# Optimization experiments

Hardware: AMD Instinct MI355X
Metric: run time of the kernel (lower is better)

Reference implementation:

```python
import jax, jax.numpy as jnp
import numpy as np

B, N, FIN, FOUT = 8, 2048, 128, 64
ALPHA = 0.2      # LeakyReLU negative slope
NEG_INF = -9e15  # matches torch constant -9000000000000000.0
LN_EPS = 1e-5


def setup_inputs() -> dict:
    key = jax.random.key(0)
    k1, k2, k3, k4 = jax.random.split(key, 4)
    x = jax.random.normal(k1, (B, N, FIN), dtype=jnp.float32)
    adj = jax.random.randint(k2, (B, N, N), 0, 2, dtype=jnp.int32)
    # params: W is nn.Linear(in,out,bias=False) -> stored here as [FIN,FOUT];
    # a is nn.Linear(2*out,1,bias=False) -> vector of length 2*FOUT.
    W = jax.random.normal(k3, (FIN, FOUT), dtype=jnp.float32) * (1.0 / np.sqrt(FIN))
    a = jax.random.normal(k4, (2 * FOUT,), dtype=jnp.float32) * (1.0 / np.sqrt(2 * FOUT))
    gamma = jnp.ones((FOUT,), dtype=jnp.float32)
    beta = jnp.zeros((FOUT,), dtype=jnp.float32)
    return {"x": x, "adj": adj, "W": W, "a": a, "gamma": gamma, "beta": beta}


def reference(x, adj, W, a, gamma, beta):
    h = jnp.einsum('bnf,fo->bno', x, W)                      # [B,N,FOUT]
    fout = h.shape[-1]
    a1, a2 = a[:fout], a[fout:]
    # a·cat(h_i,h_j) == h_i·a1 + h_j·a2 -> avoid O(N^2*2F) concat tensor
    s1 = h @ a1                                              # [B,N]
    s2 = h @ a2                                              # [B,N]
    e = jax.nn.leaky_relu(s1[:, :, None] + s2[:, None, :], ALPHA)  # [B,N,N]
    att = jnp.where(adj > 0, e, NEG_INF)
    att = jax.nn.softmax(att, axis=2)
    h_prime = jnp.einsum('bij,bjf->bif', att, h)             # [B,N,FOUT]
    # LayerNorm over last dim
    mu = jnp.mean(h_prime, axis=-1, keepdims=True)
    var = jnp.mean((h_prime - mu) ** 2, axis=-1, keepdims=True)
    y = (h_prime - mu) * jax.lax.rsqrt(var + LN_EPS) * gamma + beta
    return jax.nn.elu(y)
```

## Files before the change

### kernel.cpp

```cpp
#include <hip/hip_runtime.h>
#include <hip/hip_bf16.h>

#define B_    8
#define N_    2048
#define FIN_  128
#define FOUT_ 64
#define ALPHA_ 0.2f
#define LN_EPS_ 1e-5f

typedef __attribute__((ext_vector_type(8))) short short8;
typedef __attribute__((ext_vector_type(4))) float f32x4;

__device__ __forceinline__ short f2bf(float f) {
    __hip_bfloat16 h = __float2bfloat16(f);
    return *reinterpret_cast<short*>(&h);
}
__device__ __forceinline__ float bf2f(short s) {
    return __uint_as_float(((unsigned)(unsigned short)s) << 16);
}

__global__ __launch_bounds__(256) void k_prep(
    const float* __restrict__ W, const float* __restrict__ a,
    short* __restrict__ Wbf, float* __restrict__ Wa1g, float* __restrict__ Wa2g)
{
    const int t = threadIdx.x;
    #pragma unroll
    for (int c = 0; c < 4; ++c) {
        int g = t + 256 * c;
        int u = g >> 6, ln = g & 63;
        int ks = u >> 2, nt = u & 3;
        int n  = nt * 16 + (ln & 15);
        int k0 = ks * 32 + (ln >> 4) * 8;
        short8 v;
        #pragma unroll
        for (int jj = 0; jj < 8; ++jj) v[jj] = f2bf(W[(k0 + jj) * FOUT_ + n]);
        *(short8*)&Wbf[g * 8] = v;
    }
    if (t < FIN_) {
        float a1 = 0.f, a2 = 0.f;
        #pragma unroll
        for (int n = 0; n < FOUT_; n += 4) {
            float4 wv  = *(const float4*)&W[t * FOUT_ + n];
            float4 av1 = *(const float4*)&a[n];
            float4 av2 = *(const float4*)&a[FOUT_ + n];
            a1 += wv.x * av1.x + wv.y * av1.y + wv.z * av1.z + wv.w * av1.w;
            a2 += wv.x * av2.x + wv.y * av2.y + wv.z * av2.z + wv.w * av2.w;
        }
        Wa1g[t] = a1; Wa2g[t] = a2;
    }
}

__global__ __launch_bounds__(256) void k_proj(
    const float* __restrict__ x,
    const short* __restrict__ Wbf,
    const float* __restrict__ Wa1g, const float* __restrict__ Wa2g,
    unsigned short* __restrict__ hT,
    float* __restrict__ s1, float* __restrict__ s2)
{
    __shared__ float Wa1l[FIN_], Wa2l[FIN_];
    const int t = threadIdx.x;
    const int row0 = blockIdx.x * 32;
    const int b   = row0 >> 11;
    const int ib0 = row0 & (N_ - 1);

    if (t < FIN_) { Wa1l[t] = Wa1g[t]; Wa2l[t] = Wa2g[t]; }
    __syncthreads();

    const int wave = t >> 6, lane = t & 63;
    const int m = lane & 15, quad = lane >> 4;
    const int mt = wave & 1, nt0 = (wave >> 1) * 2;
    const int row = row0 + mt * 16 + m;

    short8 fa[4];
    float s1p = 0.f, s2p = 0.f;
    #pragma unroll
    for (int ks = 0; ks < 4; ++ks) {
        int k0 = ks * 32 + quad * 8;
        float4 x0 = *(const float4*)&x[(size_t)row * FIN_ + k0];
        float4 x1 = *(const float4*)&x[(size_t)row * FIN_ + k0 + 4];
        float xs[8] = {x0.x, x0.y, x0.z, x0.w, x1.x, x1.y, x1.z, x1.w};
        short8 v;
        #pragma unroll
        for (int jj = 0; jj < 8; ++jj) {
            v[jj] = f2bf(xs[jj]);
            s1p += xs[jj] * Wa1l[k0 + jj];
            s2p += xs[jj] * Wa2l[k0 + jj];
        }
        fa[ks] = v;
    }
    s1p += __shfl_xor(s1p, 16); s1p += __shfl_xor(s1p, 32);
    s2p += __shfl_xor(s2p, 16); s2p += __shfl_xor(s2p, 32);
    if (wave < 2 && lane < 16) {
        s1[row0 + wave * 16 + lane] = s1p;
        s2[row0 + wave * 16 + lane] = s2p;
    }

    f32x4 acc[2];
    acc[0] = (f32x4){0.f, 0.f, 0.f, 0.f};
    acc[1] = (f32x4){0.f, 0.f, 0.f, 0.f};
    #pragma unroll
    for (int ks = 0; ks < 4; ++ks) {
        #pragma unroll
        for (int q = 0; q < 2; ++q) {
            short8 fb = *(const short8*)&Wbf[((ks * 4 + nt0 + q) * 64 + lane) * 8];
            acc[q] = __builtin_amdgcn_mfma_f32_16x16x32_bf16(fa[ks], fb, acc[q], 0, 0, 0);
        }
    }
    #pragma unroll
    for (int q = 0; q < 2; ++q) {
        int o  = (nt0 + q) * 16 + m;
        int ib = ib0 + mt * 16 + quad * 4;
        ushort4 hv;
        hv.x = (unsigned short)f2bf(acc[q][0]);
        hv.y = (unsigned short)f2bf(acc[q][1]);
        hv.z = (unsigned short)f2bf(acc[q][2]);
        hv.w = (unsigned short)f2bf(acc[q][3]);
        *(ushort4*)&hT[(size_t)(b * 64 + o) * N_ + ib] = hv;
    }
}

__global__ __launch_bounds__(256) void k_attn(
    const int* __restrict__ adj,
    const unsigned short* __restrict__ hT,
    const float* __restrict__ s1g, const float* __restrict__ s2g,
    const float* __restrict__ gamma, const float* __restrict__ beta,
    float* __restrict__ out)
{
    __shared__ short Hb[16 * 64 * 8];
    __shared__ __align__(16) char pool[4096];
    __shared__ float s2l[N_];
    __shared__ float s1l[16], ml[16];
    __shared__ float lp[4][16];
    __shared__ float red[4];
    short* Wf = (short*)pool;
    float* hp = (float*)pool;

    const int t = threadIdx.x;
    const int wave = t >> 6, lane = t & 63;
    const int i_ = lane & 15, quad = lane >> 4;
    const int b  = blockIdx.x >> 7;
    const int i0 = (blockIdx.x & 127) * 16;
    const size_t sbase  = (size_t)b * N_;
    const size_t hTbase = (size_t)b * 64 * N_;

    float4 v0 = *(const float4*)&s2g[sbase + 4 * t];
    float4 v1 = *(const float4*)&s2g[sbase + 4 * (t + 256)];
    *(float4*)&s2l[4 * t] = v0;
    *(float4*)&s2l[4 * (t + 256)] = v1;
    float mx = fmaxf(fmaxf(fmaxf(v0.x, v0.y), fmaxf(v0.z, v0.w)),
                     fmaxf(fmaxf(v1.x, v1.y), fmaxf(v1.z, v1.w)));
    #pragma unroll
    for (int d = 32; d; d >>= 1) mx = fmaxf(mx, __shfl_xor(mx, d));
    if (lane == 0) red[wave] = mx;
    __syncthreads();
    {
        float smax = fmaxf(fmaxf(red[0], red[1]), fmaxf(red[2], red[3]));
        if (t < 16) {
            float s1v = s1g[sbase + i0 + t];
            s1l[t] = s1v;
            float v = s1v + smax;
            ml[t] = fmaxf(v, ALPHA_ * v);
        }
    }

    const int jr = wave * 32 + quad * 8;
    const int* adjrow = &adj[(sbase + i0 + i_) * N_ + jr];

    int4 pa0 = *(const int4*)&adjrow[0];
    int4 pa1 = *(const int4*)&adjrow[4];

    f32x4 acc = (f32x4){0.f, 0.f, 0.f, 0.f};
    float lpart = 0.f;

    for (int tile = 0; tile < 16; ++tile) {
        const int j0 = tile * 128;
        asm volatile("s_waitcnt lgkmcnt(0)\n\ts_barrier" ::: "memory");

        short8 hv[4];
        #pragma unroll
        for (int c = 0; c < 4; ++c) {
            int u  = c * 4 + wave;
            int ks = u >> 2, nt = u & 3;
            int o  = nt * 16 + i_;
            int j2 = ks * 32 + quad * 8;
            hv[c] = *(const short8*)&hT[hTbase + (size_t)o * N_ + j0 + j2];
        }

        {
            int am[8] = {pa0.x, pa0.y, pa0.z, pa0.w, pa1.x, pa1.y, pa1.z, pa1.w};
            float s1v = s1l[i_], mv = ml[i_];
            float sum = 0.f;
            short8 wv;
            #pragma unroll
            for (int jj = 0; jj < 8; ++jj) {
                float ev = s1v + s2l[j0 + jr + jj];
                ev = fmaxf(ev, ALPHA_ * ev);
                float w = (am[jj] > 0) ? __expf(ev - mv) : 0.f;
                short ws = f2bf(w);
                wv[jj] = ws;
                sum += bf2f(ws);
            }
            *(short8*)&Wf[t * 8] = wv;
            lpart += sum;
        }

        {
            int j0n = (j0 + 128) & (N_ - 1);
            pa0 = *(const int4*)&adjrow[j0n];
            pa1 = *(const int4*)&adjrow[j0n + 4];
        }

        #pragma unroll
        for (int c = 0; c < 4; ++c)
            *(short8*)&Hb[((c * 4 + wave) * 64 + lane) * 8] = hv[c];

        __syncthreads();

        #pragma unroll
        for (int ks = 0; ks < 4; ++ks) {
            short8 fa = *(short8*)&Wf[(ks * 64 + lane) * 8];
            short8 fb = *(short8*)&Hb[((ks * 4 + wave) * 64 + lane) * 8];
            acc = __builtin_amdgcn_mfma_f32_16x16x32_bf16(fa, fb, acc, 0, 0, 0);
        }
    }

    lpart += __shfl_xor(lpart, 16);
    lpart += __shfl_xor(lpart, 32);
    if (lane < 16) lp[wave][lane] = lpart;
    __syncthreads();

    {
        int col = wave * 16 + i_;
        #pragma unroll
        for (int reg = 0; reg < 4; ++reg) {
            int r = quad * 4 + reg;
            float l = lp[0][r] + lp[1][r] + lp[2][r] + lp[3][r];
            hp[r * 64 + col] = acc[reg] / l;
        }
    }
    __syncthreads();

    {
        int o = lane;
        float g  = gamma[o];
        float be = beta[o];
        #pragma unroll
        for (int rr = 0; rr < 4; ++rr) {
            int i = wave * 4 + rr;
            float v = hp[i * 64 + o];
            float mu = v;
            #pragma unroll
            for (int d = 32; d; d >>= 1) mu += __shfl_xor(mu, d);
            mu *= (1.f / 64.f);
            float dv = v - mu;
            float var = dv * dv;
            #pragma unroll
            for (int d = 32; d; d >>= 1) var += __shfl_xor(var, d);
            var *= (1.f / 64.f);
            float y = dv * rsqrtf(var + LN_EPS_) * g + be;
            out[(sbase + i0 + i) * FOUT_ + o] = y > 0.f ? y : __expf(y) - 1.f;
        }
    }
}

extern "C" void kernel_launch(void* const* d_in, const int* in_sizes, int n_in,
                              void* d_out, int out_size, void* d_ws, size_t ws_size,
                              hipStream_t stream) {
    const float* x     = (const float*)d_in[0];
    const int*   adj   = (const int*)d_in[1];
    const float* W     = (const float*)d_in[2];
    const float* a     = (const float*)d_in[3];
    const float* gamma = (const float*)d_in[4];
    const float* beta  = (const float*)d_in[5];
    float* out = (float*)d_out;

    char* ws = (char*)d_ws;
    unsigned short* hT = (unsigned short*)ws;
    float* s1   = (float*)(ws + (size_t)B_ * 64 * N_ * 2);
    float* s2   = s1 + (size_t)B_ * N_;
    short* Wbf  = (short*)(s2 + (size_t)B_ * N_);
    float* Wa1g = (float*)(Wbf + 16 * 64 * 8);
    float* Wa2g = Wa1g + FIN_;

    k_prep<<<1, 256, 0, stream>>>(W, a, Wbf, Wa1g, Wa2g);
    k_proj<<<512, 256, 0, stream>>>(x, Wbf, Wa1g, Wa2g, hT, s1, s2);
    k_attn<<<B_ * (N_ / 16), 256, 0, stream>>>(adj, hT, s1, s2, gamma, beta, out);
}
```

Measured before the change: 219.8 us.

## Pre-pack adjacency into bitmask and load mask tiles into LDS in attention

Adds a streaming kernel that compresses the int32 adjacency matrix into a 1-bit-per-edge mask. The attention kernel then loads each block's 16 mask rows into shared memory once and tests bits, instead of streaming int4 adjacency loads inside the tile loop. This takes the large adjacency reads out of the latency-sensitive attention loop, at the cost of an extra kernel launch and a full pass over adj. It also replaces the custom waitcnt barrier with __syncthreads and requires workspace past 4 MB.

```diff
diff --git a/kernel.cpp b/kernel.cpp
--- a/kernel.cpp
+++ b/kernel.cpp
@@ -17,6 +17,22 @@
 }
 __device__ __forceinline__ float bf2f(short s) {
     return __uint_as_float(((unsigned)(unsigned short)s) << 16);
+}
+
+__global__ __launch_bounds__(256) void k_pack(
+    const int* __restrict__ adj, unsigned* __restrict__ mask)
+{
+    const size_t base = ((size_t)blockIdx.x * 256 + threadIdx.x) * 32;
+    unsigned m = 0;
+    #pragma unroll
+    for (int c = 0; c < 8; ++c) {
+        int4 v = *(const int4*)&adj[base + c * 4];
+        m |= (v.x > 0 ? 1u : 0u) << (c * 4 + 0);
+        m |= (v.y > 0 ? 1u : 0u) << (c * 4 + 1);
+        m |= (v.z > 0 ? 1u : 0u) << (c * 4 + 2);
+        m |= (v.w > 0 ? 1u : 0u) << (c * 4 + 3);
+    }
+    mask[base >> 5] = m;
 }
 
 __global__ __launch_bounds__(256) void k_prep(
@@ -120,7 +136,7 @@
 }
 
 __global__ __launch_bounds__(256) void k_attn(
-    const int* __restrict__ adj,
+    const unsigned* __restrict__ maskg,
     const unsigned short* __restrict__ hT,
     const float* __restrict__ s1g, const float* __restrict__ s2g,
     const float* __restrict__ gamma, const float* __restrict__ beta,
@@ -129,6 +145,7 @@
     __shared__ short Hb[16 * 64 * 8];
     __shared__ __align__(16) char pool[4096];
     __shared__ float s2l[N_];
+    __shared__ int maskL[16 * 68];
     __shared__ float s1l[16], ml[16];
     __shared__ float lp[4][16];
     __shared__ float red[4];
@@ -143,6 +160,13 @@
     const size_t sbase  = (size_t)b * N_;
     const size_t hTbase = (size_t)b * 64 * N_;
 
+    {
+        int w4 = t * 4;
+        int r = w4 >> 6, c = w4 & 63;
+        int4 mv = *(const int4*)&maskg[(sbase + i0 + r) * (N_ / 32) + c];
+        *(int4*)&maskL[r * 68 + c] = mv;
+    }
+
     float4 v0 = *(const float4*)&s2g[sbase + 4 * t];
     float4 v1 = *(const float4*)&s2g[sbase + 4 * (t + 256)];
     *(float4*)&s2l[4 * t] = v0;
@@ -162,19 +186,15 @@
             ml[t] = fmaxf(v, ALPHA_ * v);
         }
     }
+    __syncthreads();
 
     const int jr = wave * 32 + quad * 8;
-    const int* adjrow = &adj[(sbase + i0 + i_) * N_ + jr];
-
-    int4 pa0 = *(const int4*)&adjrow[0];
-    int4 pa1 = *(const int4*)&adjrow[4];
-
     f32x4 acc = (f32x4){0.f, 0.f, 0.f, 0.f};
     float lpart = 0.f;
 
     for (int tile = 0; tile < 16; ++tile) {
         const int j0 = tile * 128;
-        asm volatile("s_waitcnt lgkmcnt(0)\n\ts_barrier" ::: "memory");
+        if (tile) __syncthreads();
 
         short8 hv[4];
         #pragma unroll
@@ -187,7 +207,7 @@
         }
 
         {
-            int am[8] = {pa0.x, pa0.y, pa0.z, pa0.w, pa1.x, pa1.y, pa1.z, pa1.w};
+            unsigned bits = ((unsigned)maskL[i_ * 68 + tile * 4 + wave]) >> (quad * 8);
             float s1v = s1l[i_], mv = ml[i_];
             float sum = 0.f;
             short8 wv;
@@ -195,19 +215,13 @@
             for (int jj = 0; jj < 8; ++jj) {
                 float ev = s1v + s2l[j0 + jr + jj];
                 ev = fmaxf(ev, ALPHA_ * ev);
-                float w = (am[jj] > 0) ? __expf(ev - mv) : 0.f;
+                float w = ((bits >> jj) & 1) ? __expf(ev - mv) : 0.f;
                 short ws = f2bf(w);
                 wv[jj] = ws;
                 sum += bf2f(ws);
             }
             *(short8*)&Wf[t * 8] = wv;
             lpart += sum;
-        }
-
-        {
-            int j0n = (j0 + 128) & (N_ - 1);
-            pa0 = *(const int4*)&adjrow[j0n];
-            pa1 = *(const int4*)&adjrow[j0n + 4];
         }
 
         #pragma unroll
@@ -281,8 +295,10 @@
     short* Wbf  = (short*)(s2 + (size_t)B_ * N_);
     float* Wa1g = (float*)(Wbf + 16 * 64 * 8);
     float* Wa2g = Wa1g + FIN_;
-
+    unsigned* maskg = (unsigned*)(ws + (4 << 20));
+
+    k_pack<<<4096, 256, 0, stream>>>(adj, maskg);
     k_prep<<<1, 256, 0, stream>>>(W, a, Wbf, Wa1g, Wa2g);
     k_proj<<<512, 256, 0, stream>>>(x, Wbf, Wa1g, Wa2g, hT, s1, s2);
-    k_attn<<<B_ * (N_ / 16), 256, 0, stream>>>(adj, hT, s1, s2, gamma, beta, out);
-}
+    k_attn<<<B_ * (N_ / 16), 256, 0, stream>>>(maskg, hT, s1, s2, gamma, beta, out);
+}
```

After: 244.1 us. 1.11x slower.

## Split attention j-range across waves and fuse weight prep into projection kernel

Applied to the files above, without the earlier changes.

The attention kernel no longer stages weights and H tiles through shared memory with two barriers per tile. Each wave now owns a slice of the key dimension, builds its own MFMA A operand from its attention weights in registers, loads H directly from global memory, and accumulates all four output column tiles. The partial results are reduced across waves in shared memory at the end. Separately, the single-block prep kernel is folded into the projection kernel, so every block recomputes the bf16 W layout and the W·a vectors itself, saving a launch at the cost of redundant work and extra shared memory.

```diff
diff --git a/kernel.cpp b/kernel.cpp
--- a/kernel.cpp
+++ b/kernel.cpp
@@ -19,11 +19,20 @@
     return __uint_as_float(((unsigned)(unsigned short)s) << 16);
 }
 
-__global__ __launch_bounds__(256) void k_prep(
-    const float* __restrict__ W, const float* __restrict__ a,
-    short* __restrict__ Wbf, float* __restrict__ Wa1g, float* __restrict__ Wa2g)
+__global__ __launch_bounds__(256) void k_proj(
+    const float* __restrict__ x,
+    const float* __restrict__ W,
+    const float* __restrict__ a,
+    unsigned short* __restrict__ hT,
+    float* __restrict__ s1, float* __restrict__ s2)
 {
+    __shared__ short Wb[16 * 64 * 8];
+    __shared__ float Wa1l[FIN_], Wa2l[FIN_];
     const int t = threadIdx.x;
+    const int row0 = blockIdx.x * 32;
+    const int b   = row0 >> 11;
+    const int ib0 = row0 & (N_ - 1);
+
     #pragma unroll
     for (int c = 0; c < 4; ++c) {
         int g = t + 256 * c;
@@ -34,7 +43,7 @@
         short8 v;
         #pragma unroll
         for (int jj = 0; jj < 8; ++jj) v[jj] = f2bf(W[(k0 + jj) * FOUT_ + n]);
-        *(short8*)&Wbf[g * 8] = v;
+        *(short8*)&Wb[g * 8] = v;
     }
     if (t < FIN_) {
         float a1 = 0.f, a2 = 0.f;
@@ -46,24 +55,8 @@
             a1 += wv.x * av1.x + wv.y * av1.y + wv.z * av1.z + wv.w * av1.w;
             a2 += wv.x * av2.x + wv.y * av2.y + wv.z * av2.z + wv.w * av2.w;
         }
-        Wa1g[t] = a1; Wa2g[t] = a2;
-    }
-}
-
-__global__ __launch_bounds__(256) void k_proj(
-    const float* __restrict__ x,
-    const short* __restrict__ Wbf,
-    const float* __restrict__ Wa1g, const float* __restrict__ Wa2g,
-    unsigned short* __restrict__ hT,
-    float* __restrict__ s1, float* __restrict__ s2)
-{
-    __shared__ float Wa1l[FIN_], Wa2l[FIN_];
-    const int t = threadIdx.x;
-    const int row0 = blockIdx.x * 32;
-    const int b   = row0 >> 11;
-    const int ib0 = row0 & (N_ - 1);
-
-    if (t < FIN_) { Wa1l[t] = Wa1g[t]; Wa2l[t] = Wa2g[t]; }
+        Wa1l[t] = a1; Wa2l[t] = a2;
+    }
     __syncthreads();
 
     const int wave = t >> 6, lane = t & 63;
@@ -102,7 +95,7 @@
     for (int ks = 0; ks < 4; ++ks) {
         #pragma unroll
         for (int q = 0; q < 2; ++q) {
-            short8 fb = *(const short8*)&Wbf[((ks * 4 + nt0 + q) * 64 + lane) * 8];
+            short8 fb = *(short8*)&Wb[((ks * 4 + nt0 + q) * 64 + lane) * 8];
             acc[q] = __builtin_amdgcn_mfma_f32_16x16x32_bf16(fa[ks], fb, acc[q], 0, 0, 0);
         }
     }
@@ -126,22 +119,18 @@
     const float* __restrict__ gamma, const float* __restrict__ beta,
     float* __restrict__ out)
 {
-    __shared__ short Hb[16 * 64 * 8];
-    __shared__ __align__(16) char pool[4096];
     __shared__ float s2l[N_];
-    __shared__ float s1l[16], ml[16];
-    __shared__ float lp[4][16];
+    __shared__ float accL[4][16][64];
+    __shared__ float lpw[4][16];
     __shared__ float red[4];
-    short* Wf = (short*)pool;
-    float* hp = (float*)pool;
 
     const int t = threadIdx.x;
     const int wave = t >> 6, lane = t & 63;
     const int i_ = lane & 15, quad = lane >> 4;
     const int b  = blockIdx.x >> 7;
     const int i0 = (blockIdx.x & 127) * 16;
-    const size_t sbase  = (size_t)b * N_;
-    const size_t hTbase = (size_t)b * 64 * N_;
+    const size_t sbase = (size_t)b * N_;
+    const size_t hTb   = (size_t)b * 64 * N_;
 
     float4 v0 = *(const float4*)&s2g[sbase + 4 * t];
     float4 v1 = *(const float4*)&s2g[sbase + 4 * (t + 256)];
@@ -153,15 +142,9 @@
     for (int d = 32; d; d >>= 1) mx = fmaxf(mx, __shfl_xor(mx, d));
     if (lane == 0) red[wave] = mx;
     __syncthreads();
-    {
-        float smax = fmaxf(fmaxf(red[0], red[1]), fmaxf(red[2], red[3]));
-        if (t < 16) {
-            float s1v = s1g[sbase + i0 + t];
-            s1l[t] = s1v;
-            float v = s1v + smax;
-            ml[t] = fmaxf(v, ALPHA_ * v);
-        }
-    }
+    const float smax = fmaxf(fmaxf(red[0], red[1]), fmaxf(red[2], red[3]));
+    const float s1v  = s1g[sbase + i0 + i_];
+    const float mv   = fmaxf(s1v + smax, ALPHA_ * (s1v + smax));
 
     const int jr = wave * 32 + quad * 8;
     const int* adjrow = &adj[(sbase + i0 + i_) * N_ + jr];
@@ -169,28 +152,28 @@
     int4 pa0 = *(const int4*)&adjrow[0];
     int4 pa1 = *(const int4*)&adjrow[4];
 
-    f32x4 acc = (f32x4){0.f, 0.f, 0.f, 0.f};
+    f32x4 acc[4];
+    #pragma unroll
+    for (int nt = 0; nt < 4; ++nt) acc[nt] = (f32x4){0.f, 0.f, 0.f, 0.f};
     float lpart = 0.f;
 
     for (int tile = 0; tile < 16; ++tile) {
         const int j0 = tile * 128;
-        asm volatile("s_waitcnt lgkmcnt(0)\n\ts_barrier" ::: "memory");
-
+        int am[8] = {pa0.x, pa0.y, pa0.z, pa0.w, pa1.x, pa1.y, pa1.z, pa1.w};
+
+        {
+            int jn = ((tile + 1) & 15) * 128;
+            pa0 = *(const int4*)&adjrow[jn];
+            pa1 = *(const int4*)&adjrow[jn + 4];
+        }
         short8 hv[4];
         #pragma unroll
-        for (int c = 0; c < 4; ++c) {
-            int u  = c * 4 + wave;
-            int ks = u >> 2, nt = u & 3;
-            int o  = nt * 16 + i_;
-            int j2 = ks * 32 + quad * 8;
-            hv[c] = *(const short8*)&hT[hTbase + (size_t)o * N_ + j0 + j2];
-        }
-
+        for (int nt = 0; nt < 4; ++nt)
+            hv[nt] = *(const short8*)&hT[hTb + (size_t)(nt * 16 + i_) * N_ + j0 + jr];
+
+        short8 wv;
         {
-            int am[8] = {pa0.x, pa0.y, pa0.z, pa0.w, pa1.x, pa1.y, pa1.z, pa1.w};
-            float s1v = s1l[i_], mv = ml[i_];
             float sum = 0.f;
-            short8 wv;
             #pragma unroll
             for (int jj = 0; jj < 8; ++jj) {
                 float ev = s1v + s2l[j0 + jr + jj];
@@ -200,54 +183,36 @@
                 wv[jj] = ws;
                 sum += bf2f(ws);
             }
-            *(short8*)&Wf[t * 8] = wv;
             lpart += sum;
         }
 
-        {
-            int j0n = (j0 + 128) & (N_ - 1);
-            pa0 = *(const int4*)&adjrow[j0n];
-            pa1 = *(const int4*)&adjrow[j0n + 4];
-        }
-
-        #pragma unroll
-        for (int c = 0; c < 4; ++c)
-            *(short8*)&Hb[((c * 4 + wave) * 64 + lane) * 8] = hv[c];
-
-        __syncthreads();
-
-        #pragma unroll
-        for (int ks = 0; ks < 4; ++ks) {
-            short8 fa = *(short8*)&Wf[(ks * 64 + lane) * 8];
-            short8 fb = *(short8*)&Hb[((ks * 4 + wave) * 64 + lane) * 8];
-            acc = __builtin_amdgcn_mfma_f32_16x16x32_bf16(fa, fb, acc, 0, 0, 0);
-        }
+        #pragma unroll
+        for (int nt = 0; nt < 4; ++nt)
+            acc[nt] = __builtin_amdgcn_mfma_f32_16x16x32_bf16(wv, hv[nt], acc[nt], 0, 0, 0);
     }
 
     lpart += __shfl_xor(lpart, 16);
     lpart += __shfl_xor(lpart, 32);
-    if (lane < 16) lp[wave][lane] = lpart;
+    if (lane < 16) lpw[wave][lane] = lpart;
+
+    #pragma unroll
+    for (int nt = 0; nt < 4; ++nt)
+        #pragma unroll
+        for (int reg = 0; reg < 4; ++reg)
+            accL[wave][nt * 4 + reg][lane] = acc[nt][reg];
     __syncthreads();
 
     {
-        int col = wave * 16 + i_;
-        #pragma unroll
-        for (int reg = 0; reg < 4; ++reg) {
-            int r = quad * 4 + reg;
-            float l = lp[0][r] + lp[1][r] + lp[2][r] + lp[3][r];
-            hp[r * 64 + col] = acc[reg] / l;
-        }
-    }
-    __syncthreads();
-
-    {
-        int o = lane;
-        float g  = gamma[o];
-        float be = beta[o];
+        const int o = lane, ntc = o >> 4, oc = o & 15;
+        const float g  = gamma[o];
+        const float be = beta[o];
         #pragma unroll
         for (int rr = 0; rr < 4; ++rr) {
             int i = wave * 4 + rr;
-            float v = hp[i * 64 + o];
+            int s = ntc * 4 + (i & 3), lp = (i >> 2) * 16 + oc;
+            float c = accL[0][s][lp] + accL[1][s][lp] + accL[2][s][lp] + accL[3][s][lp];
+            float l = lpw[0][i] + lpw[1][i] + lpw[2][i] + lpw[3][i];
+            float v = c / l;
             float mu = v;
             #pragma unroll
             for (int d = 32; d; d >>= 1) mu += __shfl_xor(mu, d);
@@ -276,13 +241,9 @@
 
     char* ws = (char*)d_ws;
     unsigned short* hT = (unsigned short*)ws;
-    float* s1   = (float*)(ws + (size_t)B_ * 64 * N_ * 2);
-    float* s2   = s1 + (size_t)B_ * N_;
-    short* Wbf  = (short*)(s2 + (size_t)B_ * N_);
-    float* Wa1g = (float*)(Wbf + 16 * 64 * 8);
-    float* Wa2g = Wa1g + FIN_;
-
-    k_prep<<<1, 256, 0, stream>>>(W, a, Wbf, Wa1g, Wa2g);
-    k_proj<<<512, 256, 0, stream>>>(x, Wbf, Wa1g, Wa2g, hT, s1, s2);
+    float* s1 = (float*)(ws + (size_t)B_ * 64 * N_ * 2);
+    float* s2 = s1 + (size_t)B_ * N_;
+
+    k_proj<<<512, 256, 0, stream>>>(x, W, a, hT, s1, s2);
     k_attn<<<B_ * (N_ / 16), 256, 0, stream>>>(adj, hT, s1, s2, gamma, beta, out);
 }
```

After: 226.3 us. 1.03x slower.
